# Optimization experiments

Hardware: AMD Instinct MI355X
Metric: run time of the kernel (lower is better)

The kernel has to match this reference:

```python
import jax, jax.numpy as jnp
import numpy as np

B, S, QD, VD, H = 32, 2048, 1024, 1024, 1024
NEG = -1e9


def setup_inputs() -> dict:
    key = jax.random.key(0)
    ks = jax.random.split(key, 7)
    query = jax.random.normal(ks[0], (B, QD), dtype=jnp.float32)
    value = jax.random.normal(ks[1], (B, S, VD), dtype=jnp.float32)
    mask = jax.random.randint(ks[2], (B, S), 0, 2).astype(bool)
    # params (Linear weights stored as [in, out] for einsum convenience)
    Wq = jax.random.normal(ks[3], (QD, H), dtype=jnp.float32) / np.sqrt(QD)
    bq = jax.random.normal(ks[4], (H,), dtype=jnp.float32) * 0.01
    Wv = jax.random.normal(ks[5], (VD, H), dtype=jnp.float32) / np.sqrt(VD)
    w = jax.random.normal(ks[6], (H,), dtype=jnp.float32) / np.sqrt(H)
    return {"query": query, "value": value, "mask": mask,
            "Wq": Wq, "bq": bq, "Wv": Wv, "w": w}


def reference(query, value, mask, Wq, bq, Wv, w):
    # q-projection: [B, H]
    hq = query @ Wq + bq
    # v-projection: [B, S, H]
    hv = jnp.einsum('bsv,vh->bsh', value, Wv)
    # additive attention energies: [B, S]
    logits = jnp.einsum('bsh,h->bs', jnp.tanh(hq[:, None, :] + hv), w)
    logits = jnp.where(mask, logits, NEG)
    return jax.nn.softmax(logits, axis=-1)
```

## Files before the change

kernel.cpp:

```cpp
#include <hip/hip_runtime.h>
#include <hip/hip_bf16.h>
#include <hip/hip_fp16.h>

typedef _Float16 f16;
typedef _Float16 f16x8 __attribute__((ext_vector_type(8)));
typedef float f32x16 __attribute__((ext_vector_type(16)));
typedef unsigned int u32;

#define BB 32
#define SS 2048
#define HH 1024
#define KK 1024

#define WS_BP 0
#define WS_HQ (2u*1024u*1024u)
#define WS_LP (WS_HQ + 131072u)

__device__ __forceinline__ float tanh_f(float x) {
    float e = __expf(2.0f * x);
    return 1.0f - 2.0f * __builtin_amdgcn_rcpf(e + 1.0f);
}

__device__ __forceinline__ void gload_lds16(const void* g, void* l) {
    __builtin_amdgcn_global_load_lds(
        (const __attribute__((address_space(1))) u32*)g,
        (__attribute__((address_space(3))) u32*)l, 16, 0, 0);
}

__global__ void pack_wv(const float* __restrict__ Wv, f16* __restrict__ BP) {
    int i = blockIdx.x * 256 + threadIdx.x;
    int k = i >> 10, n = i & 1023;
    float v = Wv[i];
    int ntb = n >> 8;
    int ntl = (n >> 5) & 7;
    int kit = k >> 5;
    int ksl = (k >> 4) & 1;
    int lane = ((k >> 3) & 1) * 32 + (n & 31);
    int j = k & 7;
    BP[((((ntb * 32 + kit) * 8 + ntl) * 2 + ksl) * 64 + lane) * 8 + j] = (f16)v;
}

__global__ void hq_kernel(const float* __restrict__ query, const float* __restrict__ Wq,
                          const float* __restrict__ bq, float* __restrict__ hq) {
    int b = blockIdx.y;
    int h = (blockIdx.x & 3) * 256 + threadIdx.x;
    int v0 = (blockIdx.x >> 2) * 256;
    float acc = 0.f;
#pragma unroll 8
    for (int v = 0; v < 256; ++v)
        acc += query[b * 1024 + v0 + v] * Wq[(v0 + v) * 1024 + h];
    if (v0 == 0) acc += bq[h];
    atomicAdd(&hq[b * 1024 + h], acc);
}

__launch_bounds__(1024, 4)
__global__ void fused_main(const float* __restrict__ value, const f16* __restrict__ BP,
                           const float* __restrict__ hq, const float* __restrict__ wvec,
                           float* __restrict__ lpart) {
    extern __shared__ char smem[];

    int bid = blockIdx.x;
    int tile = (bid & 7) * 128 + (bid >> 3);
    int Mt = tile >> 2, ntb = tile & 3;
    int m0 = Mt << 8;
    int b = m0 >> 11, s0 = m0 & 2047;

    int tid = threadIdx.x;
    int w = tid >> 6, l = tid & 63;
    int wm = w >> 2, wn = w & 3;
    int l31 = l & 31, lg = l >> 5;

    int arow = tid >> 2;
    const float* aga = value + (size_t)(m0 + arow) * 1024 + (tid & 3) * 8;
    int aw_off = arow * 64 + ((((tid & 3) ^ ((arow >> 1) & 3))) << 4);

    const char* bg = (const char*)BP + (size_t)ntb * (32u * 16384u) + tid * 16;

    int a_base[2], a_sw[2];
#pragma unroll
    for (int mt = 0; mt < 2; ++mt) {
        int row = wm * 64 + mt * 32 + l31;
        a_base[mt] = row * 64;
        a_sw[mt] = ((row >> 1) & 3) << 4;
    }
    int b_base[2];
#pragma unroll
    for (int nt = 0; nt < 2; ++nt)
        b_base[nt] = (wn * 2 + nt) * 2048 + l * 16;

    const f32x16 fzero = {};
    f32x16 acc[2][2];
#pragma unroll
    for (int mt = 0; mt < 2; ++mt)
#pragma unroll
        for (int nt = 0; nt < 2; ++nt) acc[mt][nt] = fzero;

    {
        const float4* ap = (const float4*)aga;
        float4 fa0 = ap[0], fa1 = ap[1];
        gload_lds16(bg, smem + 32768 + tid * 16);
        union { f16 h[8]; uint4 u; } pk;
        pk.h[0] = (f16)fa0.x; pk.h[1] = (f16)fa0.y; pk.h[2] = (f16)fa0.z; pk.h[3] = (f16)fa0.w;
        pk.h[4] = (f16)fa1.x; pk.h[5] = (f16)fa1.y; pk.h[6] = (f16)fa1.z; pk.h[7] = (f16)fa1.w;
        *(uint4*)(smem + aw_off) = pk.u;
        __syncthreads();
    }

#pragma unroll 1
    for (int t = 0; t < 32; ++t) {
        const char* Acur = smem + (t & 1) * 16384;
        const char* Bcur = smem + 32768 + (t & 1) * 16384;
        char* Anx = smem + ((t + 1) & 1) * 16384;
        char* Bnx = smem + 32768 + ((t + 1) & 1) * 16384;

        float4 fa0, fa1;
        if (t < 31) {
            const float4* ap = (const float4*)(aga + (t + 1) * 32);
            fa0 = ap[0]; fa1 = ap[1];
            gload_lds16(bg + (size_t)(t + 1) * 16384, Bnx + tid * 16);
        }

#pragma unroll
        for (int ks = 0; ks < 2; ++ks) {
            int sl = (ks * 2 + lg) << 4;
            f16x8 av0 = *(const f16x8*)(Acur + a_base[0] + (sl ^ a_sw[0]));
            f16x8 av1 = *(const f16x8*)(Acur + a_base[1] + (sl ^ a_sw[1]));
            f16x8 bv0 = *(const f16x8*)(Bcur + b_base[0] + ks * 1024);
            f16x8 bv1 = *(const f16x8*)(Bcur + b_base[1] + ks * 1024);
            acc[0][0] = __builtin_amdgcn_mfma_f32_32x32x16_f16(av0, bv0, acc[0][0], 0, 0, 0);
            acc[0][1] = __builtin_amdgcn_mfma_f32_32x32x16_f16(av0, bv1, acc[0][1], 0, 0, 0);
            acc[1][0] = __builtin_amdgcn_mfma_f32_32x32x16_f16(av1, bv0, acc[1][0], 0, 0, 0);
            acc[1][1] = __builtin_amdgcn_mfma_f32_32x32x16_f16(av1, bv1, acc[1][1], 0, 0, 0);
        }

        if (t < 31) {
            union { f16 h[8]; uint4 u; } pk;
            pk.h[0] = (f16)fa0.x; pk.h[1] = (f16)fa0.y; pk.h[2] = (f16)fa0.z; pk.h[3] = (f16)fa0.w;
            pk.h[4] = (f16)fa1.x; pk.h[5] = (f16)fa1.y; pk.h[6] = (f16)fa1.z; pk.h[7] = (f16)fa1.w;
            *(uint4*)(Anx + aw_off) = pk.u;
        }
        __syncthreads();
    }

    int h0 = ntb * 256 + wn * 64 + l31;
    int h1 = h0 + 32;
    float hq0 = hq[b * 1024 + h0], hq1 = hq[b * 1024 + h1];
    float w0 = wvec[h0], w1 = wvec[h1];

    float* part = (float*)smem;
#pragma unroll
    for (int mt = 0; mt < 2; ++mt) {
#pragma unroll
        for (int r = 0; r < 16; ++r) {
            float p = tanh_f(hq0 + acc[mt][0][r]) * w0
                    + tanh_f(hq1 + acc[mt][1][r]) * w1;
            p += __shfl_xor(p, 1); p += __shfl_xor(p, 2); p += __shfl_xor(p, 4);
            p += __shfl_xor(p, 8); p += __shfl_xor(p, 16);
            if (l31 == 0) {
                int row = wm * 64 + mt * 32 + (r & 3) + ((r >> 2) << 3) + (lg << 2);
                part[wn * 256 + row] = p;
            }
        }
    }
    __syncthreads();
    if (tid < 256) {
        float s = part[tid] + part[256 + tid] + part[512 + tid] + part[768 + tid];
        lpart[((size_t)ntb * 32 + b) * 2048 + s0 + tid] = s;
    }
}

__global__ void softmax_kernel(const float* __restrict__ lp, const int* __restrict__ mask,
                               float* __restrict__ out) {
    __shared__ float redm[16];
    __shared__ float reds[16];
    const int P = 32 * 2048;
    int b = blockIdx.x, t = threadIdx.x;
    int wid = t >> 6, lane = t & 63;
    int i0 = b * 2048 + t, i1 = i0 + 1024;
    float l0 = lp[i0] + lp[P + i0] + lp[2 * P + i0] + lp[3 * P + i0];
    float l1 = lp[i1] + lp[P + i1] + lp[2 * P + i1] + lp[3 * P + i1];
    float a0 = mask[i0] ? l0 : -1e9f;
    float a1 = mask[i1] ? l1 : -1e9f;
    float mx = fmaxf(a0, a1);
#pragma unroll
    for (int off = 1; off < 64; off <<= 1) mx = fmaxf(mx, __shfl_xor(mx, off));
    if (lane == 0) redm[wid] = mx;
    __syncthreads();
    mx = redm[0];
#pragma unroll
    for (int i = 1; i < 16; ++i) mx = fmaxf(mx, redm[i]);
    float e0 = __expf(a0 - mx), e1 = __expf(a1 - mx);
    float s = e0 + e1;
#pragma unroll
    for (int off = 1; off < 64; off <<= 1) s += __shfl_xor(s, off);
    if (lane == 0) reds[wid] = s;
    __syncthreads();
    float tot = 0.f;
#pragma unroll
    for (int i = 0; i < 16; ++i) tot += reds[i];
    float inv = 1.0f / tot;
    out[b * 2048 + t] = e0 * inv;
    out[b * 2048 + 1024 + t] = e1 * inv;
}

extern "C" void kernel_launch(void* const* d_in, const int* in_sizes, int n_in,
                              void* d_out, int out_size, void* d_ws, size_t ws_size,
                              hipStream_t stream) {
    const float* query = (const float*)d_in[0];
    const float* value = (const float*)d_in[1];
    const int*   mask  = (const int*)d_in[2];
    const float* Wq    = (const float*)d_in[3];
    const float* bq    = (const float*)d_in[4];
    const float* Wv    = (const float*)d_in[5];
    const float* wv    = (const float*)d_in[6];

    char* ws = (char*)d_ws;
    f16*   BP    = (f16*)(ws + WS_BP);
    float* hq    = (float*)(ws + WS_HQ);
    float* lpart = (float*)(ws + WS_LP);
    float* out   = (float*)d_out;

    hipMemsetAsync(hq, 0, BB * HH * sizeof(float), stream);
    pack_wv<<<(KK * HH) / 256, 256, 0, stream>>>(Wv, BP);
    hq_kernel<<<dim3(16, BB), 256, 0, stream>>>(query, Wq, bq, hq);
    fused_main<<<1024, 1024, 65536, stream>>>(value, BP, hq, wv, lpart);
    softmax_kernel<<<BB, 1024, 0, stream>>>(lpart, mask, out);
}
```

Before: 237.7 us.

## Drop LDS staging in main GEMM; load A/B fragments directly into registers

Measured after the change: 575.0 us. 142% more time.

```diff
diff --git a/kernel.cpp b/kernel.cpp
--- a/kernel.cpp
+++ b/kernel.cpp
@@ -21,10 +21,11 @@
     return 1.0f - 2.0f * __builtin_amdgcn_rcpf(e + 1.0f);
 }
 
-__device__ __forceinline__ void gload_lds16(const void* g, void* l) {
-    __builtin_amdgcn_global_load_lds(
-        (const __attribute__((address_space(1))) u32*)g,
-        (__attribute__((address_space(3))) u32*)l, 16, 0, 0);
+__device__ __forceinline__ f16x8 cvt8(float4 va, float4 vb) {
+    union { f16 h[8]; f16x8 v; } u;
+    u.h[0] = (f16)va.x; u.h[1] = (f16)va.y; u.h[2] = (f16)va.z; u.h[3] = (f16)va.w;
+    u.h[4] = (f16)vb.x; u.h[5] = (f16)vb.y; u.h[6] = (f16)vb.z; u.h[7] = (f16)vb.w;
+    return u.v;
 }
 
 __global__ void pack_wv(const float* __restrict__ Wv, f16* __restrict__ BP) {
@@ -53,40 +54,24 @@
     atomicAdd(&hq[b * 1024 + h], acc);
 }
 
-__launch_bounds__(1024, 4)
+__launch_bounds__(256, 3)
 __global__ void fused_main(const float* __restrict__ value, const f16* __restrict__ BP,
                            const float* __restrict__ hq, const float* __restrict__ wvec,
                            float* __restrict__ lpart) {
-    extern __shared__ char smem[];
+    __shared__ float part[256];
 
     int bid = blockIdx.x;
-    int tile = (bid & 7) * 128 + (bid >> 3);
+    int tile = (bid & 7) * 512 + (bid >> 3);
     int Mt = tile >> 2, ntb = tile & 3;
-    int m0 = Mt << 8;
+    int m0 = Mt << 6;
     int b = m0 >> 11, s0 = m0 & 2047;
 
     int tid = threadIdx.x;
-    int w = tid >> 6, l = tid & 63;
-    int wm = w >> 2, wn = w & 3;
+    int wn = tid >> 6, l = tid & 63;
     int l31 = l & 31, lg = l >> 5;
 
-    int arow = tid >> 2;
-    const float* aga = value + (size_t)(m0 + arow) * 1024 + (tid & 3) * 8;
-    int aw_off = arow * 64 + ((((tid & 3) ^ ((arow >> 1) & 3))) << 4);
-
-    const char* bg = (const char*)BP + (size_t)ntb * (32u * 16384u) + tid * 16;
-
-    int a_base[2], a_sw[2];
-#pragma unroll
-    for (int mt = 0; mt < 2; ++mt) {
-        int row = wm * 64 + mt * 32 + l31;
-        a_base[mt] = row * 64;
-        a_sw[mt] = ((row >> 1) & 3) << 4;
-    }
-    int b_base[2];
-#pragma unroll
-    for (int nt = 0; nt < 2; ++nt)
-        b_base[nt] = (wn * 2 + nt) * 2048 + l * 16;
+    const float* aA = value + (size_t)(m0 + l31) * 1024 + lg * 8;
+    const char* bB = (const char*)BP + (size_t)ntb * 524288 + (wn * 2) * 2048 + (size_t)l * 16;
 
     const f32x16 fzero = {};
     f32x16 acc[2][2];
@@ -95,51 +80,39 @@
 #pragma unroll
         for (int nt = 0; nt < 2; ++nt) acc[mt][nt] = fzero;
 
-    {
-        const float4* ap = (const float4*)aga;
-        float4 fa0 = ap[0], fa1 = ap[1];
-        gload_lds16(bg, smem + 32768 + tid * 16);
-        union { f16 h[8]; uint4 u; } pk;
-        pk.h[0] = (f16)fa0.x; pk.h[1] = (f16)fa0.y; pk.h[2] = (f16)fa0.z; pk.h[3] = (f16)fa0.w;
-        pk.h[4] = (f16)fa1.x; pk.h[5] = (f16)fa1.y; pk.h[6] = (f16)fa1.z; pk.h[7] = (f16)fa1.w;
-        *(uint4*)(smem + aw_off) = pk.u;
-        __syncthreads();
-    }
-
 #pragma unroll 1
     for (int t = 0; t < 32; ++t) {
-        const char* Acur = smem + (t & 1) * 16384;
-        const char* Bcur = smem + 32768 + (t & 1) * 16384;
-        char* Anx = smem + ((t + 1) & 1) * 16384;
-        char* Bnx = smem + 32768 + ((t + 1) & 1) * 16384;
-
-        float4 fa0, fa1;
-        if (t < 31) {
-            const float4* ap = (const float4*)(aga + (t + 1) * 32);
-            fa0 = ap[0]; fa1 = ap[1];
-            gload_lds16(bg + (size_t)(t + 1) * 16384, Bnx + tid * 16);
-        }
-
-#pragma unroll
-        for (int ks = 0; ks < 2; ++ks) {
-            int sl = (ks * 2 + lg) << 4;
-            f16x8 av0 = *(const f16x8*)(Acur + a_base[0] + (sl ^ a_sw[0]));
-            f16x8 av1 = *(const f16x8*)(Acur + a_base[1] + (sl ^ a_sw[1]));
-            f16x8 bv0 = *(const f16x8*)(Bcur + b_base[0] + ks * 1024);
-            f16x8 bv1 = *(const f16x8*)(Bcur + b_base[1] + ks * 1024);
-            acc[0][0] = __builtin_amdgcn_mfma_f32_32x32x16_f16(av0, bv0, acc[0][0], 0, 0, 0);
-            acc[0][1] = __builtin_amdgcn_mfma_f32_32x32x16_f16(av0, bv1, acc[0][1], 0, 0, 0);
-            acc[1][0] = __builtin_amdgcn_mfma_f32_32x32x16_f16(av1, bv0, acc[1][0], 0, 0, 0);
-            acc[1][1] = __builtin_amdgcn_mfma_f32_32x32x16_f16(av1, bv1, acc[1][1], 0, 0, 0);
-        }
-
-        if (t < 31) {
-            union { f16 h[8]; uint4 u; } pk;
-            pk.h[0] = (f16)fa0.x; pk.h[1] = (f16)fa0.y; pk.h[2] = (f16)fa0.z; pk.h[3] = (f16)fa0.w;
-            pk.h[4] = (f16)fa1.x; pk.h[5] = (f16)fa1.y; pk.h[6] = (f16)fa1.z; pk.h[7] = (f16)fa1.w;
-            *(uint4*)(Anx + aw_off) = pk.u;
-        }
-        __syncthreads();
+        float4 ax[2][2], ay[2][2];
+        const float* at = aA + t * 32;
+#pragma unroll
+        for (int mt = 0; mt < 2; ++mt)
+#pragma unroll
+            for (int ks = 0; ks < 2; ++ks) {
+                const float4* p = (const float4*)(at + mt * 32768 + ks * 16);
+                ax[mt][ks] = p[0];
+                ay[mt][ks] = p[1];
+            }
+        const f16x8* bp = (const f16x8*)(bB + (size_t)t * 16384);
+        f16x8 bv[2][2];
+#pragma unroll
+        for (int nt = 0; nt < 2; ++nt)
+#pragma unroll
+            for (int ks = 0; ks < 2; ++ks)
+                bv[nt][ks] = bp[nt * 128 + ks * 64];
+        f16x8 av[2][2];
+#pragma unroll
+        for (int mt = 0; mt < 2; ++mt)
+#pragma unroll
+            for (int ks = 0; ks < 2; ++ks)
+                av[mt][ks] = cvt8(ax[mt][ks], ay[mt][ks]);
+#pragma unroll
+        for (int ks = 0; ks < 2; ++ks)
+#pragma unroll
+            for (int mt = 0; mt < 2; ++mt)
+#pragma unroll
+                for (int nt = 0; nt < 2; ++nt)
+                    acc[mt][nt] = __builtin_amdgcn_mfma_f32_32x32x16_f16(
+                        av[mt][ks], bv[nt][ks], acc[mt][nt], 0, 0, 0);
     }
 
     int h0 = ntb * 256 + wn * 64 + l31;
@@ -147,24 +120,28 @@
     float hq0 = hq[b * 1024 + h0], hq1 = hq[b * 1024 + h1];
     float w0 = wvec[h0], w1 = wvec[h1];
 
-    float* part = (float*)smem;
 #pragma unroll
     for (int mt = 0; mt < 2; ++mt) {
 #pragma unroll
-        for (int r = 0; r < 16; ++r) {
-            float p = tanh_f(hq0 + acc[mt][0][r]) * w0
-                    + tanh_f(hq1 + acc[mt][1][r]) * w1;
-            p += __shfl_xor(p, 1); p += __shfl_xor(p, 2); p += __shfl_xor(p, 4);
-            p += __shfl_xor(p, 8); p += __shfl_xor(p, 16);
-            if (l31 == 0) {
-                int row = wm * 64 + mt * 32 + (r & 3) + ((r >> 2) << 3) + (lg << 2);
-                part[wn * 256 + row] = p;
+        for (int i = 0; i < 8; ++i) {
+            float pa = tanh_f(hq0 + acc[mt][0][2 * i]) * w0
+                     + tanh_f(hq1 + acc[mt][1][2 * i]) * w1;
+            float pb = tanh_f(hq0 + acc[mt][0][2 * i + 1]) * w0
+                     + tanh_f(hq1 + acc[mt][1][2 * i + 1]) * w1;
+            float ea = __shfl_xor(pa, 1), eb = __shfl_xor(pb, 1);
+            float g = (l & 1) ? (pb + eb) : (pa + ea);
+            g += __shfl_xor(g, 2); g += __shfl_xor(g, 4);
+            g += __shfl_xor(g, 8); g += __shfl_xor(g, 16);
+            if (l31 < 2) {
+                int r = 2 * i + (l31 & 1);
+                int row = mt * 32 + (r & 3) + ((r >> 2) << 3) + (lg << 2);
+                part[wn * 64 + row] = g;
             }
         }
     }
     __syncthreads();
-    if (tid < 256) {
-        float s = part[tid] + part[256 + tid] + part[512 + tid] + part[768 + tid];
+    if (tid < 64) {
+        float s = part[tid] + part[64 + tid] + part[128 + tid] + part[192 + tid];
         lpart[((size_t)ntb * 32 + b) * 2048 + s0 + tid] = s;
     }
 }
@@ -220,9 +197,9 @@
     float* lpart = (float*)(ws + WS_LP);
     float* out   = (float*)d_out;
 
-    hipMemsetAsync(hq, 0, BB * HH * sizeof(float), stream);
+    (void)hipMemsetAsync(hq, 0, BB * HH * sizeof(float), stream);
     pack_wv<<<(KK * HH) / 256, 256, 0, stream>>>(Wv, BP);
     hq_kernel<<<dim3(16, BB), 256, 0, stream>>>(query, Wq, bq, hq);
-    fused_main<<<1024, 1024, 65536, stream>>>(value, BP, hq, wv, lpart);
+    fused_main<<<4096, 256, 0, stream>>>(value, BP, hq, wv, lpart);
     softmax_kernel<<<BB, 1024, 0, stream>>>(lpart, mask, out);
 }
```
